# Performance work log

Hardware: AMD Instinct MI355X
Metric: run time of the kernel (lower is better)

## Reference

```python
import jax, jax.numpy as jnp
import numpy as np

B, L, D = 2, 2048, 2048
H, KVH, HD, FD = 8, 1, 256, 64   # heads, kv heads, head_dim, feature_dim
CHUNK = 64


def setup_inputs() -> dict:
    key = jax.random.key(0)
    ks = jax.random.split(key, 8)
    hidden_states = jax.random.normal(ks[0], (B, L, D), dtype=jnp.float32)
    # Gemma-style RoPE tables over half the head dim
    half = HD // 2
    inv_freq = 1.0 / (10000.0 ** (jnp.arange(half, dtype=jnp.float32) / half))
    ang = jnp.arange(L, dtype=jnp.float32)[:, None] * inv_freq[None, :]  # [L, half]
    freqs_cos, freqs_sin = jnp.cos(ang), jnp.sin(ang)
    mask = jnp.ones((1, 1, L, L), dtype=bool)  # unused in linear path
    s = 0.02
    Wq = jax.random.normal(ks[1], (D, H * HD), dtype=jnp.float32) * s
    Wk = jax.random.normal(ks[2], (D, KVH * HD), dtype=jnp.float32) * s
    Wv = jax.random.normal(ks[3], (D, KVH * HD), dtype=jnp.float32) * s
    Wo = jax.random.normal(ks[4], (H * HD, D), dtype=jnp.float32) * s
    fmq = jax.random.normal(ks[5], (H, HD, FD), dtype=jnp.float32) * s
    fmk = jax.random.normal(ks[6], (H, HD, FD), dtype=jnp.float32) * s
    return dict(hidden_states=hidden_states, freqs_cos=freqs_cos, freqs_sin=freqs_sin,
                mask=mask, Wq=Wq, Wk=Wk, Wv=Wv, Wo=Wo, fmq=fmq, fmk=fmk)


def _rope(x, cos, sin):
    # x: [B, L, h, HD]; Gemma complex RoPE: first half = real, second half = imag
    half = x.shape[-1] // 2
    x1, x2 = x[..., :half], x[..., half:]
    c = cos[None, :, None, :]
    s = sin[None, :, None, :]
    return jnp.concatenate([x1 * c - x2 * s, x1 * s + x2 * c], axis=-1)


def _hedgehog(x, W):
    # x: [B, H, L, HD], W: [H, HD, FD] -> softmax over cat([xW, -xW]) -> [B,H,L,2*FD]
    p = jnp.einsum('bhld,hdf->bhlf', x, W)
    return jax.nn.softmax(jnp.concatenate([p, -p], axis=-1), axis=-1)


def _chunk_linear_attn(q, k, v, chunk=CHUNK):
    # q,k: [B,H,L,F]; v: [B,H,L,HD]; chunked causal linear attention
    b, h, l, f = q.shape
    dv = v.shape[-1]
    n = l // chunk
    q = q.reshape(b, h, n, chunk, f) * (f ** -0.5)
    k = k.reshape(b, h, n, chunk, f)
    v = v.reshape(b, h, n, chunk, dv)
    kv = jnp.einsum('bhncf,bhncd->bhnfd', k, v)            # per-chunk KV
    kv = jnp.cumsum(kv, axis=2)
    kv = jnp.concatenate([jnp.zeros_like(kv[:, :, :1]), kv[:, :, :-1]], axis=2)  # exclusive prefix
    inter = jnp.einsum('bhncf,bhnfd->bhncd', q, kv)        # cross-chunk term
    s = jnp.einsum('bhnif,bhnjf->bhnij', q, k)             # intra-chunk scores
    tri = jnp.tril(jnp.ones((chunk, chunk), dtype=bool))
    s = jnp.where(tri, s, 0.0)
    intra = jnp.einsum('bhnij,bhnjd->bhnid', s, v)
    return (inter + intra).reshape(b, h, l, dv)


def reference(hidden_states, freqs_cos, freqs_sin, mask, Wq, Wk, Wv, Wo, fmq, fmk):
    b, l, _ = hidden_states.shape
    q = (hidden_states @ Wq).reshape(b, l, H, HD)
    k = (hidden_states @ Wk).reshape(b, l, KVH, HD)
    v = (hidden_states @ Wv).reshape(b, l, KVH, HD)
    q = _rope(q, freqs_cos, freqs_sin)
    k = _rope(k, freqs_cos, freqs_sin)
    # repeat_interleave kv heads to num_heads (MQA expansion)
    rep = H // KVH
    k = jnp.repeat(k, rep, axis=2)
    v = jnp.repeat(v, rep, axis=2)
    q = jnp.transpose(q, (0, 2, 1, 3))  # [B,H,L,HD]
    k = jnp.transpose(k, (0, 2, 1, 3))
    v = jnp.transpose(v, (0, 2, 1, 3))
    q = _hedgehog(q, fmq)
    k = _hedgehog(k, fmk)
    o = _chunk_linear_attn(q, k, v)                         # [B,H,L,HD]
    o = jnp.transpose(o, (0, 2, 1, 3)).reshape(b, l, H * HD)
    return o @ Wo
```

## Files before the change

### kernel.cpp

```cpp
#include <hip/hip_runtime.h>

#define B_ 2
#define L_ 2048
#define D_ 2048
#define H_ 8
#define HD_ 256
#define FD_ 64
#define F_ 128
#define NC_ 32
#define M_ (B_*L_)
#define SCALE_Q 0.08838834764831845f

typedef unsigned short u16;
typedef __attribute__((ext_vector_type(8))) short bf16x8;
typedef __attribute__((ext_vector_type(8))) unsigned short u16x8;
typedef __attribute__((ext_vector_type(16))) float f32x16;
typedef __attribute__((ext_vector_type(4))) unsigned int u32x4;

#define FMA4(a_, s_, v_) { (a_).x += (s_)*(v_).x; (a_).y += (s_)*(v_).y; \
                           (a_).z += (s_)*(v_).z; (a_).w += (s_)*(v_).w; }


__device__ __forceinline__ u16 bf16_rne(float x) {
  unsigned u = __float_as_uint(x);
  return (u16)((u + 0x7fffu + ((u >> 16) & 1u)) >> 16);
}
__device__ __forceinline__ void bf16_split(float x, u16& h, u16& l) {
  unsigned u = __float_as_uint(x);
  unsigned hb = (u + 0x7fffu + ((u >> 16) & 1u)) >> 16;
  h = (u16)hb;
  float hf = __uint_as_float(hb << 16);
  l = bf16_rne(x - hf);
}

__device__ __forceinline__ void gl_lds16(const u16* g, u16* l) {
  __builtin_amdgcn_global_load_lds(
      (const __attribute__((address_space(1))) unsigned int*)g,
      (__attribute__((address_space(3))) unsigned int*)l, 16, 0, 0);
}

__device__ __forceinline__ size_t kvb_off(int d, int f) {
  return (size_t)(((d >> 7) & 1) * 16384 + ((f >> 5) & 3) * 4096 +
                  ((d >> 6) & 1) * 2048 + ((f >> 4) & 1) * 1024 +
                  ((d >> 5) & 1) * 512 + ((f >> 3) & 1) * 256 +
                  (d & 31) * 8 + (f & 7));
}
__device__ __forceinline__ size_t vb_off(int d, int j) {
  return (size_t)(((d >> 7) & 1) * 8192 + ((j >> 5) & 1) * 4096 +
                  ((d >> 6) & 1) * 2048 + ((j >> 4) & 1) * 1024 +
                  ((d >> 5) & 1) * 512 + ((j >> 3) & 1) * 256 +
                  (d & 31) * 8 + (j & 7));
}

__device__ __forceinline__ void wtrans_body(const float* __restrict__ W, int Nsrc,
                                            int n0, u16* __restrict__ dst,
                                            int P, int kt) {
  int t = threadIdx.x;
  int nn = t & 127, kh = t >> 7;
  const float* src = W + (size_t)(kt * 32 + kh * 16) * Nsrc + n0 + nn;
  u16x8 u0, u1;
  #pragma unroll
  for (int kk = 0; kk < 8; ++kk) u0[kk] = bf16_rne(src[(size_t)kk * Nsrc]);
  #pragma unroll
  for (int kk = 0; kk < 8; ++kk) u1[kk] = bf16_rne(src[(size_t)(kk + 8) * Nsrc]);
  size_t base = ((size_t)P * 64 + kt) * 4096 + (size_t)((nn >> 6) & 1) * 2048
              + (size_t)kh * 1024 + (size_t)((nn >> 5) & 1) * 512
              + (size_t)(nn & 31) * 8;
  *(u16x8*)(dst + base) = u0;
  *(u16x8*)(dst + base + 256) = u1;
}

__global__ __launch_bounds__(256)
void prep_kernel(const float* __restrict__ hs,
                 const float* __restrict__ Wq, const float* __restrict__ Wk,
                 const float* __restrict__ Wv, const float* __restrict__ Wo,
                 u16* __restrict__ hsHt, u16* __restrict__ hsLt,
                 u16* __restrict__ WTh, u16* __restrict__ WoTh) {
  int bid = blockIdx.x;
  if (bid < 4096) {
    int gid = bid * 256 + threadIdx.x;
    int r = gid >> 8, u = gid & 255;
    const float* src = hs + (size_t)r * 2048 + u * 8;
    float4 v0 = *(const float4*)src, v1 = *(const float4*)(src + 4);
    float vals[8] = {v0.x, v0.y, v0.z, v0.w, v1.x, v1.y, v1.z, v1.w};
    u16x8 hv, lv;
    #pragma unroll
    for (int j = 0; j < 8; ++j) { u16 hh, ll; bf16_split(vals[j], hh, ll); hv[j] = hh; lv[j] = ll; }
    size_t off = ((size_t)(r >> 6) * 64 + (u >> 2)) * 2048
               + (size_t)((u >> 1) & 1) * 1024 + (size_t)((r >> 5) & 1) * 512
               + (size_t)(u & 1) * 256 + (size_t)(r & 31) * 8;
    *(u16x8*)(hsHt + off) = hv;
    *(u16x8*)(hsLt + off) = lv;
  } else if (bid < 5376) {
    int idx = bid - 4096;
    int P = idx >> 6, kt = idx & 63;
    const float* W; int Nsrc, n0;
    if (P < 16)      { W = Wq; Nsrc = 2048; n0 = P * 128; }
    else if (P < 18) { W = Wk; Nsrc = 256;  n0 = (P - 16) * 128; }
    else             { W = Wv; Nsrc = 256;  n0 = (P - 18) * 128; }
    wtrans_body(W, Nsrc, n0, WTh, P, kt);
  } else {
    int idx = bid - 5376;
    wtrans_body(Wo, 2048, (idx >> 6) * 128, WoTh, idx >> 6, idx & 63);
  }
}

__global__ __launch_bounds__(256)
void wtrans_wo(const float* __restrict__ Wo, u16* __restrict__ WoTh) {
  wtrans_body(Wo, 2048, blockIdx.x * 128, WoTh, blockIdx.x, blockIdx.y);
}

__device__ __forceinline__ void mfma_body(
    const u16* __restrict__ AtH, const u16* __restrict__ AtL,
    const u16* __restrict__ Bt, float* __restrict__ C, int cstride,
    int bm, int bn) {
  __shared__ __align__(16) u16 AsH[2048];
  __shared__ __align__(16) u16 AsL[2048];
  __shared__ __align__(16) u16 Bs[4096];
  const int t = threadIdx.x, lane = t & 63, wv = t >> 6;
  const u16* aSrc = (wv ? AtL : AtH) + (size_t)bm * 131072 + lane * 8;
  const u16* bSrc = Bt + (size_t)bn * 262144 + wv * 2048 + lane * 8;
  u16* aDst = wv ? AsL : AsH;
  u16* bDst = Bs + wv * 2048;

  f32x16 acc[2][2];
  #pragma unroll
  for (int a = 0; a < 2; ++a)
    #pragma unroll
    for (int b2 = 0; b2 < 2; ++b2)
      #pragma unroll
      for (int r = 0; r < 16; ++r) acc[a][b2][r] = 0.f;

  for (int kt = 0; kt < 64; ++kt) {
    const u16* ak = aSrc + (size_t)kt * 2048;
    const u16* bk = bSrc + (size_t)kt * 4096;
    __syncthreads();
    #pragma unroll
    for (int c = 0; c < 4; ++c) {
      gl_lds16(ak + c * 512, aDst + c * 512);
      gl_lds16(bk + c * 512, bDst + c * 512);
    }
    __syncthreads();

    #pragma unroll
    for (int ks = 0; ks < 2; ++ks) {
      const u16* ph = AsH + ks * 1024 + lane * 8;
      const u16* pl = AsL + ks * 1024 + lane * 8;
      const u16* pb = Bs + wv * 2048 + ks * 1024 + lane * 8;
      bf16x8 a0 = *(const bf16x8*)ph;
      bf16x8 a1 = *(const bf16x8*)(ph + 512);
      bf16x8 b0 = *(const bf16x8*)pb;
      bf16x8 b1 = *(const bf16x8*)(pb + 512);
      acc[0][0] = __builtin_amdgcn_mfma_f32_32x32x16_bf16(a0, b0, acc[0][0], 0, 0, 0);
      acc[0][1] = __builtin_amdgcn_mfma_f32_32x32x16_bf16(a0, b1, acc[0][1], 0, 0, 0);
      acc[1][0] = __builtin_amdgcn_mfma_f32_32x32x16_bf16(a1, b0, acc[1][0], 0, 0, 0);
      acc[1][1] = __builtin_amdgcn_mfma_f32_32x32x16_bf16(a1, b1, acc[1][1], 0, 0, 0);
      bf16x8 l0 = *(const bf16x8*)pl;
      bf16x8 l1 = *(const bf16x8*)(pl + 512);
      acc[0][0] = __builtin_amdgcn_mfma_f32_32x32x16_bf16(l0, b0, acc[0][0], 0, 0, 0);
      acc[0][1] = __builtin_amdgcn_mfma_f32_32x32x16_bf16(l0, b1, acc[0][1], 0, 0, 0);
      acc[1][0] = __builtin_amdgcn_mfma_f32_32x32x16_bf16(l1, b0, acc[1][0], 0, 0, 0);
      acc[1][1] = __builtin_amdgcn_mfma_f32_32x32x16_bf16(l1, b1, acc[1][1], 0, 0, 0);
    }
  }

  const int fr = lane & 31, g = lane >> 5;
  float* Cp = C + (size_t)(bm * 64) * cstride + wv * 64;
  #pragma unroll
  for (int mt = 0; mt < 2; ++mt)
    #pragma unroll
    for (int nt = 0; nt < 2; ++nt) {
      #pragma unroll
      for (int r = 0; r < 16; ++r) {
        int row = mt * 32 + (r & 3) + 8 * (r >> 2) + 4 * g;
        Cp[(size_t)row * cstride + nt * 32 + fr] = acc[mt][nt][r];
      }
    }
}

#define SUB_ 12288
#define MFB(a_, b_, c_) (c_) = __builtin_amdgcn_mfma_f32_32x32x16_bf16((a_), (b_), (c_), 0, 0, 0)

__device__ __forceinline__ void mfma_big_body(
    const u16* __restrict__ AtH, const u16* __restrict__ AtL,
    const u16* __restrict__ Bt, float* __restrict__ C, int cstride,
    int bm, int bn) {
  __shared__ __align__(16) u16 lds[3 * SUB_];
  const int t = threadIdx.x, lane = t & 63, wv = t >> 6;
  const int wm = wv >> 1, wn = wv & 1;

  const u16* gs[6];
  unsigned lo[6], gst[6];
  #pragma unroll
  for (int j = 0; j < 6; ++j) {
    int line = wv * 6 + j;
    if (line < 8) {
      gs[j] = AtH + ((size_t)(2 * bm + (line >> 2)) * 64) * 2048
                  + (size_t)(line & 3) * 512 + lane * 8;
      gst[j] = 2048;
    } else if (line < 16) {
      int l2 = line - 8;
      gs[j] = AtL + ((size_t)(2 * bm + (l2 >> 2)) * 64) * 2048
                  + (size_t)(l2 & 3) * 512 + lane * 8;
      gst[j] = 2048;
    } else {
      int l3 = line - 16;
      gs[j] = Bt + (size_t)bn * 262144 + (size_t)l3 * 512 + lane * 8;
      gst[j] = 4096;
    }
    lo[j] = line * 512;
  }

  f32x16 acc[2][2];
  #pragma unroll
  for (int a = 0; a < 2; ++a)
    #pragma unroll
    for (int b2 = 0; b2 < 2; ++b2)
      #pragma unroll
      for (int r = 0; r < 16; ++r) acc[a][b2][r] = 0.f;

  #pragma unroll
  for (int j = 0; j < 6; ++j) gl_lds16(gs[j], lds + lo[j]);
  #pragma unroll
  for (int j = 0; j < 6; ++j) gl_lds16(gs[j] + gst[j], lds + SUB_ + lo[j]);
  asm volatile("s_waitcnt vmcnt(6)" ::: "memory");
  __builtin_amdgcn_s_barrier();
  __builtin_amdgcn_sched_barrier(0);

  int cb = 0;
  for (int kt = 0; kt < 64; ++kt) {
    int sb = cb + 2 * SUB_; if (sb >= 3 * SUB_) sb -= 3 * SUB_;
    const u16* base = lds + cb;
    const u16* ph0 = base + wm * 2048 + lane * 8;
    const u16* pb0 = base + 8192 + wn * 2048 + lane * 8;

    bf16x8 a0 = *(const bf16x8*)(ph0);
    bf16x8 a1 = *(const bf16x8*)(ph0 + 512);
    bf16x8 l0 = *(const bf16x8*)(ph0 + 4096);
    bf16x8 l1 = *(const bf16x8*)(ph0 + 4608);
    bf16x8 b0 = *(const bf16x8*)(pb0);
    bf16x8 b1 = *(const bf16x8*)(pb0 + 512);
    if (kt < 62) {
      gl_lds16(gs[0] + (size_t)(kt + 2) * gst[0], lds + sb + lo[0]);
      gl_lds16(gs[1] + (size_t)(kt + 2) * gst[1], lds + sb + lo[1]);
      gl_lds16(gs[2] + (size_t)(kt + 2) * gst[2], lds + sb + lo[2]);
    }
    __builtin_amdgcn_s_barrier();
    asm volatile("s_waitcnt lgkmcnt(0)" ::: "memory");
    __builtin_amdgcn_sched_barrier(0);
    __builtin_amdgcn_s_setprio(1);
    MFB(a0, b0, acc[0][0]); MFB(a0, b1, acc[0][1]);
    MFB(a1, b0, acc[1][0]); MFB(a1, b1, acc[1][1]);
    MFB(l0, b0, acc[0][0]); MFB(l0, b1, acc[0][1]);
    MFB(l1, b0, acc[1][0]); MFB(l1, b1, acc[1][1]);
    __builtin_amdgcn_s_setprio(0);
    __builtin_amdgcn_s_barrier();
    __builtin_amdgcn_sched_barrier(0);

    bf16x8 c0 = *(const bf16x8*)(ph0 + 1024);
    bf16x8 c1 = *(const bf16x8*)(ph0 + 1536);
    bf16x8 m0 = *(const bf16x8*)(ph0 + 5120);
    bf16x8 m1 = *(const bf16x8*)(ph0 + 5632);
    bf16x8 d0 = *(const bf16x8*)(pb0 + 1024);
    bf16x8 d1 = *(const bf16x8*)(pb0 + 1536);
    if (kt < 62) {
      gl_lds16(gs[3] + (size_t)(kt + 2) * gst[3], lds + sb + lo[3]);
      gl_lds16(gs[4] + (size_t)(kt + 2) * gst[4], lds + sb + lo[4]);
      gl_lds16(gs[5] + (size_t)(kt + 2) * gst[5], lds + sb + lo[5]);
    }
    __builtin_amdgcn_s_barrier();
    asm volatile("s_waitcnt lgkmcnt(0)" ::: "memory");
    __builtin_amdgcn_sched_barrier(0);
    __builtin_amdgcn_s_setprio(1);
    MFB(c0, d0, acc[0][0]); MFB(c0, d1, acc[0][1]);
    MFB(c1, d0, acc[1][0]); MFB(c1, d1, acc[1][1]);
    MFB(m0, d0, acc[0][0]); MFB(m0, d1, acc[0][1]);
    MFB(m1, d0, acc[1][0]); MFB(m1, d1, acc[1][1]);
    __builtin_amdgcn_s_setprio(0);
    if (kt < 62) asm volatile("s_waitcnt vmcnt(6)" ::: "memory");
    else         asm volatile("s_waitcnt vmcnt(0)" ::: "memory");
    __builtin_amdgcn_s_barrier();
    __builtin_amdgcn_sched_barrier(0);
    cb += SUB_; if (cb == 3 * SUB_) cb = 0;
  }

  const int fr = lane & 31, g = lane >> 5;
  float* Cp = C + (size_t)(bm * 128 + wm * 64) * cstride + wn * 64;
  #pragma unroll
  for (int mt = 0; mt < 2; ++mt)
    #pragma unroll
    for (int nt = 0; nt < 2; ++nt) {
      #pragma unroll
      for (int r = 0; r < 16; ++r) {
        int row = mt * 32 + (r & 3) + 8 * (r >> 2) + 4 * g;
        Cp[(size_t)row * cstride + nt * 32 + fr] = acc[mt][nt][r];
      }
    }
}

__global__ __launch_bounds__(256, 2)
void mfma_q(const u16* __restrict__ hsHt, const u16* __restrict__ hsLt,
            const u16* __restrict__ WTh, float* __restrict__ q) {
  mfma_big_body(hsHt, hsLt, WTh, q + blockIdx.x * 128, 2048,
                blockIdx.y, blockIdx.x);
}

__global__ __launch_bounds__(128, 4)
void mfma_kv(const u16* __restrict__ hsHt, const u16* __restrict__ hsLt,
             const u16* __restrict__ WTh,
             float* __restrict__ k, float* __restrict__ v) {
  int bn = blockIdx.x;
  float* Cb; int co;
  if (bn < 2) { Cb = k; co = bn * 128; }
  else        { Cb = v; co = (bn - 2) * 128; }
  mfma_body(hsHt, hsLt, WTh, Cb + co, 256, blockIdx.y, 16 + bn);
}

__global__ __launch_bounds__(256, 2)
void mfma_wo(const u16* __restrict__ oHt, const u16* __restrict__ oLt,
             const u16* __restrict__ WoTh, float* __restrict__ out) {
  mfma_big_body(oHt, oLt, WoTh, out + blockIdx.x * 128, 2048,
                blockIdx.y, blockIdx.x);
}

__device__ __forceinline__ float wave_max64(float v) {
  #pragma unroll
  for (int off = 32; off > 0; off >>= 1) v = fmaxf(v, __shfl_xor(v, off, 64));
  return v;
}
__device__ __forceinline__ float wave_sum64(float v) {
  #pragma unroll
  for (int off = 32; off > 0; off >>= 1) v += __shfl_xor(v, off, 64);
  return v;
}

__global__ __launch_bounds__(256)
void hedgehog_kernel(const float* __restrict__ q, const float* __restrict__ kx,
                     const float* __restrict__ fmq, const float* __restrict__ fmk,
                     const float* __restrict__ cosb, const float* __restrict__ sinb,
                     float* __restrict__ qf, float* __restrict__ kf,
                     const float* __restrict__ vsrc,
                     u16* __restrict__ vbH, u16* __restrict__ vbL) {
  int bid = blockIdx.x;
  if (bid >= 4096) {
    int bn = bid - 4096;
    const float* vp = vsrc + (size_t)bn * 64 * HD_;
    size_t cbout = (size_t)bn * 16384;
    int d = threadIdx.x;
    #pragma unroll
    for (int it = 0; it < 8; ++it) {
      int j0 = it * 8;
      u16x8 hv, lv;
      #pragma unroll
      for (int c = 0; c < 8; ++c) {
        u16 hh, ll; bf16_split(vp[(size_t)(j0 + c) * HD_ + d], hh, ll);
        hv[c] = hh; lv[c] = ll;
      }
      size_t off = cbout + vb_off(d, j0);
      *(u16x8*)(vbH + off) = hv;
      *(u16x8*)(vbL + off) = lv;
    }
    return;
  }
  __shared__ __align__(16) float rows[4][4][256];
  const float* x; const float* fm; float* out; int nh_in, gb;
  if (bid < 2048) { x = q;  fm = fmq; out = qf; nh_in = 8; gb = bid * 4; }
  else            { x = kx; fm = fmk; out = kf; nh_in = 1; gb = (bid - 2048) * 4; }
  int wave = threadIdx.x >> 6, lane = threadIdx.x & 63;
  int g = gb + wave;
  int l4 = g & (L_/4 - 1);
  int bh = g / (L_/4);
  int h = bh & 7, b = bh >> 3;
  int l0 = l4 * 4;
  size_t rstride = (nh_in == 1) ? (size_t)HD_ : (size_t)H_ * HD_;
  const float* xrow = (nh_in == 1)
      ? x + (size_t)(b * L_ + l0) * HD_
      : x + ((size_t)(b * L_ + l0) * H_ + h) * HD_;
  int dd = (lane & 31) * 4;
  #pragma unroll
  for (int r = 0; r < 4; ++r) {
    float4 v = *(const float4*)(xrow + r * rstride + lane * 4);
    float4 u;
    u.x = __shfl_xor(v.x, 32, 64); u.y = __shfl_xor(v.y, 32, 64);
    u.z = __shfl_xor(v.z, 32, 64); u.w = __shfl_xor(v.w, 32, 64);
    int l = l0 + r;
    float4 c = *(const float4*)(cosb + (size_t)l * 128 + dd);
    float4 s = *(const float4*)(sinb + (size_t)l * 128 + dd);
    float4 ro;
    if (lane < 32) {
      ro.x = v.x * c.x - u.x * s.x; ro.y = v.y * c.y - u.y * s.y;
      ro.z = v.z * c.z - u.z * s.z; ro.w = v.w * c.w - u.w * s.w;
    } else {
      ro.x = u.x * s.x + v.x * c.x; ro.y = u.y * s.y + v.y * c.y;
      ro.z = u.z * s.z + v.z * c.z; ro.w = u.w * s.w + v.w * c.w;
    }
    *(float4*)&rows[wave][r][lane * 4] = ro;
  }
  __syncthreads();

  const float* fmh = fm + (size_t)h * HD_ * FD_;
  float p0 = 0.f, p1 = 0.f, p2 = 0.f, p3 = 0.f;
  for (int d2 = 0; d2 < HD_; d2 += 4) {
    float w0 = fmh[(d2 + 0) * FD_ + lane];
    float w1 = fmh[(d2 + 1) * FD_ + lane];
    float w2 = fmh[(d2 + 2) * FD_ + lane];
    float w3 = fmh[(d2 + 3) * FD_ + lane];
    float4 r0 = *(const float4*)&rows[wave][0][d2];
    float4 r1 = *(const float4*)&rows[wave][1][d2];
    float4 r2 = *(const float4*)&rows[wave][2][d2];
    float4 r3 = *(const float4*)&rows[wave][3][d2];
    p0 += r0.x * w0 + r0.y * w1 + r0.z * w2 + r0.w * w3;
    p1 += r1.x * w0 + r1.y * w1 + r1.z * w2 + r1.w * w3;
    p2 += r2.x * w0 + r2.y * w1 + r2.z * w2 + r2.w * w3;
    p3 += r3.x * w0 + r3.y * w1 + r3.z * w2 + r3.w * w3;
  }
  float p[4] = {p0, p1, p2, p3};
  #pragma unroll
  for (int r = 0; r < 4; ++r) {
    float m = wave_max64(fabsf(p[r]));
    float e1 = __expf(p[r] - m);
    float e2 = __expf(-p[r] - m);
    float z = wave_sum64(e1 + e2);
    float inv = 1.0f / z;
    size_t base = ((size_t)bh * L_ + l0 + r) * F_;
    out[base + lane]      = e1 * inv;
    out[base + 64 + lane] = e2 * inv;
  }
}

__global__ __launch_bounds__(256)
void chunk_kv_kernel(const float* __restrict__ kf, const float* __restrict__ v,
                     u16* __restrict__ kvbH, u16* __restrict__ kvbL) {
  __shared__ __align__(16) float kfs[64][128];
  int n = blockIdx.x & (NC_ - 1), bh = blockIdx.x >> 5;
  int b = bh >> 3;
  const float* kfp = kf + ((size_t)bh * L_ + (size_t)n * 64) * F_;
  int t = threadIdx.x;
  #pragma unroll
  for (int it = 0; it < 8; ++it) {
    int flat = t * 4 + it * 1024;
    *(float4*)&kfs[flat >> 7][flat & 127] = *(const float4*)(kfp + flat);
  }
  __syncthreads();
  int dg = t & 63;
  int fg = t >> 6;
  const float* vp = v + (size_t)(b * L_ + n * 64) * HD_ + dg * 4;
  size_t cb = (size_t)blockIdx.x * 32768;
  #pragma unroll
  for (int pass = 0; pass < 4; ++pass) {
    int f0 = fg * 8 + pass * 32;
    float4 acc[8];
    #pragma unroll
    for (int i = 0; i < 8; ++i) acc[i] = make_float4(0.f, 0.f, 0.f, 0.f);
    for (int j = 0; j < 64; ++j) {
      float4 vv = *(const float4*)(vp + (size_t)j * HD_);
      float4 ka = *(const float4*)&kfs[j][f0];
      float4 kb = *(const float4*)&kfs[j][f0 + 4];
      FMA4(acc[0], ka.x, vv); FMA4(acc[1], ka.y, vv);
      FMA4(acc[2], ka.z, vv); FMA4(acc[3], ka.w, vv);
      FMA4(acc[4], kb.x, vv); FMA4(acc[5], kb.y, vv);
      FMA4(acc[6], kb.z, vv); FMA4(acc[7], kb.w, vv);
    }
    #pragma unroll
    for (int c = 0; c < 4; ++c) {
      u16x8 hv, lv;
      #pragma unroll
      for (int ff = 0; ff < 8; ++ff) {
        float xs = (c == 0) ? acc[ff].x : (c == 1) ? acc[ff].y
                 : (c == 2) ? acc[ff].z : acc[ff].w;
        u16 hh, ll; bf16_split(xs, hh, ll); hv[ff] = hh; lv[ff] = ll;
      }
      int d = dg * 4 + c;
      size_t off = cb + kvb_off(d, f0);
      *(u16x8*)(kvbH + off) = hv;
      *(u16x8*)(kvbL + off) = lv;
    }
  }
}

__global__ __launch_bounds__(256)
void chunk_scan_kernel(u16* __restrict__ kvbH, u16* __restrict__ kvbL) {
  int bh = blockIdx.x >> 4, g = blockIdx.x & 15;
  int d = threadIdx.x;
  size_t off = kvb_off(d, g * 8);
  float run[8] = {0.f, 0.f, 0.f, 0.f, 0.f, 0.f, 0.f, 0.f};
  for (int n = 0; n < NC_; ++n) {
    size_t a = ((size_t)(bh * 32 + n)) * 32768 + off;
    u16x8 hv = *(u16x8*)(kvbH + a);
    u16x8 lv = *(u16x8*)(kvbL + a);
    u16x8 oh, ol;
    #pragma unroll
    for (int c = 0; c < 8; ++c) {
      float val = __uint_as_float((unsigned)hv[c] << 16)
                + __uint_as_float((unsigned)lv[c] << 16);
      u16 hh, ll; bf16_split(run[c], hh, ll); oh[c] = hh; ol[c] = ll;
      run[c] += val;
    }
    *(u16x8*)(kvbH + a) = oh;
    *(u16x8*)(kvbL + a) = ol;
  }
}

__global__ __launch_bounds__(256, 2)
void chunk_attn_kernel(const float* __restrict__ qf, const float* __restrict__ kf,
                       const u16* __restrict__ vbH, const u16* __restrict__ vbL,
                       const u16* __restrict__ kvbH, const u16* __restrict__ kvbL,
                       u16* __restrict__ oHt, u16* __restrict__ oLt) {
  __shared__ __align__(16) u16 lds[32768];
  const int n = blockIdx.x & (NC_ - 1), bh = blockIdx.x >> 5;
  const int h = bh & 7, b = bh >> 3;
  const int t = threadIdx.x;
  const int w = t >> 6, i31 = t & 31, G = (t >> 5) & 1;
  const int l8 = (t & 63) * 8;

  {
    const float* qp = qf + ((size_t)bh * L_ + (size_t)n * 64) * F_;
    const float* kp = kf + ((size_t)bh * L_ + (size_t)n * 64) * F_;
    int o8 = t & 15, ib = t >> 4;
    #pragma unroll
    for (int iter = 0; iter < 4; ++iter) {
      int i = ib + iter * 16;
      int it = i >> 5, ks = o8 >> 1;
      int sub = (it * 8 + ks) * 512 + (o8 & 1) * 256 + (i & 31) * 8;
      {
        const float* src = qp + (size_t)i * 128 + o8 * 8;
        float4 a = *(const float4*)src, c = *(const float4*)(src + 4);
        float vals[8] = {a.x, a.y, a.z, a.w, c.x, c.y, c.z, c.w};
        u16x8 hv, lv;
        #pragma unroll
        for (int j = 0; j < 8; ++j) {
          u16 hh, ll; bf16_split(vals[j] * SCALE_Q, hh, ll);
          hv[j] = hh; lv[j] = ll;
        }
        *(u16x8*)(lds + sub) = hv;
        *(u16x8*)(lds + 8192 + sub) = lv;
      }
      {
        const float* src = kp + (size_t)i * 128 + o8 * 8;
        float4 a = *(const float4*)src, c = *(const float4*)(src + 4);
        float vals[8] = {a.x, a.y, a.z, a.w, c.x, c.y, c.z, c.w};
        u16x8 hv, lv;
        #pragma unroll
        for (int j = 0; j < 8; ++j) {
          u16 hh, ll; bf16_split(vals[j], hh, ll);
          hv[j] = hh; lv[j] = ll;
        }
        *(u16x8*)(lds + 16384 + sub) = hv;
        *(u16x8*)(lds + 24576 + sub) = lv;
      }
    }
  }
  __syncthreads();

  const u16* Lq  = lds;
  const u16* Lql = lds + 8192;
  const u16* Lk  = lds + 16384;
  const u16* Lkl = lds + 24576;

  f32x16 st[2][2];
  #pragma unroll
  for (int a = 0; a < 2; ++a)
    #pragma unroll
    for (int c = 0; c < 2; ++c)
      #pragma unroll
      for (int r = 0; r < 16; ++r) st[a][c][r] = 0.f;

  #pragma unroll
  for (int ks = 0; ks < 8; ++ks) {
    bf16x8 kh0 = *(const bf16x8*)(Lk  + ks * 512 + l8);
    bf16x8 kh1 = *(const bf16x8*)(Lk  + (8 + ks) * 512 + l8);
    bf16x8 kl0 = *(const bf16x8*)(Lkl + ks * 512 + l8);
    bf16x8 kl1 = *(const bf16x8*)(Lkl + (8 + ks) * 512 + l8);
    bf16x8 qh0 = *(const bf16x8*)(Lq  + ks * 512 + l8);
    bf16x8 qh1 = *(const bf16x8*)(Lq  + (8 + ks) * 512 + l8);
    bf16x8 ql0 = *(const bf16x8*)(Lql + ks * 512 + l8);
    bf16x8 ql1 = *(const bf16x8*)(Lql + (8 + ks) * 512 + l8);
    MFB(kh0, qh0, st[0][0]); MFB(kh0, ql0, st[0][0]); MFB(kl0, qh0, st[0][0]);
    MFB(kh0, qh1, st[0][1]); MFB(kh0, ql1, st[0][1]); MFB(kl0, qh1, st[0][1]);
    MFB(kh1, qh0, st[1][0]); MFB(kh1, ql0, st[1][0]); MFB(kl1, qh0, st[1][0]);
    MFB(kh1, qh1, st[1][1]); MFB(kh1, ql1, st[1][1]); MFB(kl1, qh1, st[1][1]);
  }

  bf16x8 sfH[2][4], sfL[2][4];
  #pragma unroll
  for (int mt = 0; mt < 2; ++mt) {
    int iv = mt * 32 + i31;
    #pragma unroll
    for (int ksj = 0; ksj < 4; ++ksj) {
      const int jt = ksj >> 1, kb = ksj & 1;
      unsigned ph[4], pl[4];
      #pragma unroll
      for (int half = 0; half < 2; ++half) {
        u16 hh[4], ll[4];
        #pragma unroll
        for (int c = 0; c < 4; ++c) {
          int r = 8 * kb + 4 * half + c;
          int jv = jt * 32 + (r & 3) + 8 * (r >> 2) + 4 * G;
          float mv = (jv <= iv) ? st[jt][mt][r] : 0.f;
          u16 h_, l_; bf16_split(mv, h_, l_);
          hh[c] = h_; ll[c] = l_;
        }
        ph[half * 2 + 0] = (unsigned)hh[0] | ((unsigned)hh[1] << 16);
        ph[half * 2 + 1] = (unsigned)hh[2] | ((unsigned)hh[3] << 16);
        pl[half * 2 + 0] = (unsigned)ll[0] | ((unsigned)ll[1] << 16);
        pl[half * 2 + 1] = (unsigned)ll[2] | ((unsigned)ll[3] << 16);
      }
      unsigned rH1 = (unsigned)__shfl_xor((int)(G ? ph[0] : ph[2]), 32, 64);
      unsigned rH2 = (unsigned)__shfl_xor((int)(G ? ph[1] : ph[3]), 32, 64);
      unsigned rL1 = (unsigned)__shfl_xor((int)(G ? pl[0] : pl[2]), 32, 64);
      unsigned rL2 = (unsigned)__shfl_xor((int)(G ? pl[1] : pl[3]), 32, 64);
      u32x4 wH, wL;
      wH[0] = G ? rH1 : ph[0]; wH[1] = G ? rH2 : ph[1];
      wH[2] = G ? ph[2] : rH1; wH[3] = G ? ph[3] : rH2;
      wL[0] = G ? rL1 : pl[0]; wL[1] = G ? rL2 : pl[1];
      wL[2] = G ? pl[2] : rL1; wL[3] = G ? pl[3] : rL2;
      sfH[mt][ksj] = __builtin_bit_cast(bf16x8, wH);
      sfL[mt][ksj] = __builtin_bit_cast(bf16x8, wL);
    }
  }

  f32x16 acc[2][2];
  #pragma unroll
  for (int a = 0; a < 2; ++a)
    #pragma unroll
    for (int c = 0; c < 2; ++c)
      #pragma unroll
      for (int r = 0; r < 16; ++r) acc[a][c][r] = 0.f;

  {
    size_t vcb = ((size_t)(b * NC_ + n)) * 16384;
    #pragma unroll
    for (int nt = 0; nt < 2; ++nt) {
      #pragma unroll
      for (int ksj = 0; ksj < 4; ++ksj) {
        size_t basev = vcb + vb_off(w * 64 + nt * 32, ksj * 16) + l8;
        bf16x8 vH = *(const bf16x8*)((const short*)(vbH + basev));
        bf16x8 vL = *(const bf16x8*)((const short*)(vbL + basev));
        MFB(sfH[0][ksj], vH, acc[0][nt]); MFB(sfL[0][ksj], vH, acc[0][nt]);
        MFB(sfH[0][ksj], vL, acc[0][nt]);
        MFB(sfH[1][ksj], vH, acc[1][nt]); MFB(sfL[1][ksj], vH, acc[1][nt]);
        MFB(sfH[1][ksj], vL, acc[1][nt]);
      }
    }
  }

  {
    size_t cb = (size_t)blockIdx.x * 32768;
    #pragma unroll
    for (int ks = 0; ks < 8; ++ks) {
      bf16x8 qa_h0 = *(const bf16x8*)(Lq  + ks * 512 + l8);
      bf16x8 qa_h1 = *(const bf16x8*)(Lq  + (8 + ks) * 512 + l8);
      bf16x8 qa_l0 = *(const bf16x8*)(Lql + ks * 512 + l8);
      bf16x8 qa_l1 = *(const bf16x8*)(Lql + (8 + ks) * 512 + l8);
      #pragma unroll
      for (int nt = 0; nt < 2; ++nt) {
        size_t base = cb + kvb_off(w * 64 + nt * 32, ks * 16) + l8;
        bf16x8 kvH = *(const bf16x8*)((const short*)(kvbH + base));
        bf16x8 kvL = *(const bf16x8*)((const short*)(kvbL + base));
        MFB(qa_h0, kvH, acc[0][nt]); MFB(qa_l0, kvH, acc[0][nt]);
        MFB(qa_h0, kvL, acc[0][nt]);
        MFB(qa_h1, kvH, acc[1][nt]); MFB(qa_l1, kvH, acc[1][nt]);
        MFB(qa_h1, kvL, acc[1][nt]);
      }
    }
  }

  {
    int p = b * NC_ + n;
    #pragma unroll
    for (int mt = 0; mt < 2; ++mt)
      #pragma unroll
      for (int nt = 0; nt < 2; ++nt) {
        int u_ = h * 32 + w * 8 + nt * 4 + (i31 >> 3);
        size_t ob = ((size_t)p * 64 + (u_ >> 2)) * 2048
                  + (size_t)((u_ >> 1) & 1) * 1024 + (size_t)mt * 512
                  + (size_t)(u_ & 1) * 256 + (size_t)(i31 & 7);
        #pragma unroll
        for (int r = 0; r < 16; ++r) {
          int rr = (r & 3) + 8 * (r >> 2) + 4 * G;
          u16 hh, ll; bf16_split(acc[mt][nt][r], hh, ll);
          oHt[ob + (size_t)rr * 8] = hh;
          oLt[ob + (size_t)rr * 8] = ll;
        }
      }
  }
}

extern "C" void kernel_launch(void* const* d_in, const int* in_sizes, int n_in,
                              void* d_out, int out_size, void* d_ws, size_t ws_size,
                              hipStream_t stream) {
  const float* hs   = (const float*)d_in[0];
  const float* fcos = (const float*)d_in[1];
  const float* fsin = (const float*)d_in[2];
  const float* Wq  = (const float*)d_in[4];
  const float* Wk  = (const float*)d_in[5];
  const float* Wv  = (const float*)d_in[6];
  const float* Wo  = (const float*)d_in[7];
  const float* fmq = (const float*)d_in[8];
  const float* fmk = (const float*)d_in[9];
  float* out = (float*)d_out;

  float* ws = (float*)d_ws;
  float* q  = ws;
  float* k  = q  + (size_t)M_ * 2048;
  float* v  = k  + (size_t)M_ * 256;
  float* qf = v  + (size_t)M_ * 256;
  float* kf = qf + (size_t)B_ * H_ * L_ * F_;
  float* kvr = kf + (size_t)B_ * H_ * L_ * F_;

  u16* hsHt = (u16*)kvr;
  u16* hsLt = hsHt + (size_t)M_ * 2048;
  u16* WTh  = hsLt + (size_t)M_ * 2048;
  u16* kvbH = (u16*)kvr;
  u16* kvbL = kvbH + (size_t)512 * 32768;
  u16* vbH  = (u16*)k;
  u16* vbL  = vbH + (size_t)64 * 16384;
  u16* oHt  = (u16*)q;
  u16* oLt  = oHt + (size_t)M_ * 2048;

  const size_t WS_BASE = (size_t)142606336;
  bool bigws = ws_size >= WS_BASE + (size_t)8388608;
  u16* WoTh = bigws ? (u16*)((char*)d_ws + WS_BASE) : (u16*)kvr;

  prep_kernel<<<bigws ? 6400 : 5376, 256, 0, stream>>>(
      hs, Wq, Wk, Wv, Wo, hsHt, hsLt, WTh, WoTh);
  mfma_q<<<dim3(16, 32), 256, 0, stream>>>(hsHt, hsLt, WTh, q);
  mfma_kv<<<dim3(4, 64), 128, 0, stream>>>(hsHt, hsLt, WTh, k, v);
  hedgehog_kernel<<<4096 + 64, 256, 0, stream>>>(q, k, fmq, fmk, fcos, fsin,
                                                 qf, kf, v, vbH, vbL);
  chunk_kv_kernel<<<B_ * H_ * NC_, 256, 0, stream>>>(kf, v, kvbH, kvbL);
  chunk_scan_kernel<<<256, 256, 0, stream>>>(kvbH, kvbL);
  chunk_attn_kernel<<<B_ * H_ * NC_, 256, 0, stream>>>(qf, kf, vbH, vbL,
                                                       kvbH, kvbL, oHt, oLt);
  if (!bigws)
    wtrans_wo<<<dim3(16, 64), 256, 0, stream>>>(Wo, WoTh);
  mfma_wo<<<dim3(16, 32), 256, 0, stream>>>(oHt, oLt, WoTh, out);
}
```

Baseline: 490.2 us.

## Compute hedgehog feature-map projection with split-bf16 MFMA instead of scalar FMAs

Replaces the scalar hedgehog kernel, where each wave handled four rows with per-lane FMA loops, with an MFMA kernel. Each block does RoPE on 128 rows, splits them into hi/lo bf16 in LDS, and multiplies by pre-split feature-map weights using three bf16 MFMAs to keep near-fp32 accuracy. The softmax then runs across 32-lane groups on the accumulator layout. The feature-map weights are pre-transposed and split in prep_kernel. The v bf16 conversion moves to a separate workspace region so it does not alias k, with a fallback kernel when the workspace is small. The block count drops from 4096 to 512 with a large 128KB LDS footprint, which limits occupancy.

```diff
diff --git a/kernel.cpp b/kernel.cpp
--- a/kernel.cpp
+++ b/kernel.cpp
@@ -14,6 +14,7 @@
 typedef unsigned short u16;
 typedef __attribute__((ext_vector_type(8))) short bf16x8;
 typedef __attribute__((ext_vector_type(8))) unsigned short u16x8;
+typedef __attribute__((ext_vector_type(4))) unsigned short u16x4;
 typedef __attribute__((ext_vector_type(16))) float f32x16;
 typedef __attribute__((ext_vector_type(4))) unsigned int u32x4;
 
@@ -74,8 +75,10 @@
 void prep_kernel(const float* __restrict__ hs,
                  const float* __restrict__ Wq, const float* __restrict__ Wk,
                  const float* __restrict__ Wv, const float* __restrict__ Wo,
+                 const float* __restrict__ fmq, const float* __restrict__ fmk,
                  u16* __restrict__ hsHt, u16* __restrict__ hsLt,
-                 u16* __restrict__ WTh, u16* __restrict__ WoTh) {
+                 u16* __restrict__ WTh, u16* __restrict__ WoTh,
+                 u16* __restrict__ fmbtH, u16* __restrict__ fmbtL) {
   int bid = blockIdx.x;
   if (bid < 4096) {
     int gid = bid * 256 + threadIdx.x;
@@ -99,8 +102,26 @@
     else if (P < 18) { W = Wk; Nsrc = 256;  n0 = (P - 16) * 128; }
     else             { W = Wv; Nsrc = 256;  n0 = (P - 18) * 128; }
     wtrans_body(W, Nsrc, n0, WTh, P, kt);
+  } else if (bid < 5504) {
+    int idx = bid - 5376;
+    int h16 = idx >> 3, kt = idx & 7;
+    const float* src = (h16 < 8) ? (fmq + (size_t)h16 * 16384)
+                                 : (fmk + (size_t)(h16 - 8) * 16384);
+    int t = threadIdx.x;
+    int f = t & 63, kq = t >> 6;
+    u16x8 hv, lv;
+    #pragma unroll
+    for (int i = 0; i < 8; ++i) {
+      float val = src[(size_t)(kt * 32 + kq * 8 + i) * 64 + f];
+      u16 hh, ll; bf16_split(val, hh, ll); hv[i] = hh; lv[i] = ll;
+    }
+    size_t base = (size_t)(h16 * 8 + kt) * 2048 + (size_t)(kq >> 1) * 1024
+                + (size_t)(f >> 5) * 512 + (size_t)(kq & 1) * 256
+                + (size_t)(f & 31) * 8;
+    *(u16x8*)(fmbtH + base) = hv;
+    *(u16x8*)(fmbtL + base) = lv;
   } else {
-    int idx = bid - 5376;
+    int idx = bid - 5504;
     wtrans_body(Wo, 2048, (idx >> 6) * 128, WoTh, idx >> 6, idx & 63);
   }
 }
@@ -108,6 +129,28 @@
 __global__ __launch_bounds__(256)
 void wtrans_wo(const float* __restrict__ Wo, u16* __restrict__ WoTh) {
   wtrans_body(Wo, 2048, blockIdx.x * 128, WoTh, blockIdx.x, blockIdx.y);
+}
+
+__global__ __launch_bounds__(256)
+void prep_v(const float* __restrict__ v, u16* __restrict__ vbH,
+            u16* __restrict__ vbL) {
+  int bn = blockIdx.x;
+  const float* vp = v + (size_t)bn * 64 * HD_;
+  size_t cbout = (size_t)bn * 16384;
+  int d = threadIdx.x;
+  #pragma unroll
+  for (int it = 0; it < 8; ++it) {
+    int j0 = it * 8;
+    u16x8 hv, lv;
+    #pragma unroll
+    for (int c = 0; c < 8; ++c) {
+      u16 hh, ll; bf16_split(vp[(size_t)(j0 + c) * HD_ + d], hh, ll);
+      hv[c] = hh; lv[c] = ll;
+    }
+    size_t off = cbout + vb_off(d, j0);
+    *(u16x8*)(vbH + off) = hv;
+    *(u16x8*)(vbL + off) = lv;
+  }
 }
 
 __device__ __forceinline__ void mfma_body(
@@ -323,27 +366,16 @@
                 blockIdx.y, blockIdx.x);
 }
 
-__device__ __forceinline__ float wave_max64(float v) {
-  #pragma unroll
-  for (int off = 32; off > 0; off >>= 1) v = fmaxf(v, __shfl_xor(v, off, 64));
-  return v;
-}
-__device__ __forceinline__ float wave_sum64(float v) {
-  #pragma unroll
-  for (int off = 32; off > 0; off >>= 1) v += __shfl_xor(v, off, 64);
-  return v;
-}
-
-__global__ __launch_bounds__(256)
-void hedgehog_kernel(const float* __restrict__ q, const float* __restrict__ kx,
-                     const float* __restrict__ fmq, const float* __restrict__ fmk,
-                     const float* __restrict__ cosb, const float* __restrict__ sinb,
-                     float* __restrict__ qf, float* __restrict__ kf,
-                     const float* __restrict__ vsrc,
-                     u16* __restrict__ vbH, u16* __restrict__ vbL) {
+__global__ __launch_bounds__(256, 1)
+void mfma_hh(const float* __restrict__ q, const float* __restrict__ kx,
+             const float* __restrict__ cosb, const float* __restrict__ sinb,
+             const u16* __restrict__ fmbtH, const u16* __restrict__ fmbtL,
+             float* __restrict__ qf, float* __restrict__ kf,
+             const float* __restrict__ vsrc,
+             u16* __restrict__ vbH, u16* __restrict__ vbL) {
   int bid = blockIdx.x;
-  if (bid >= 4096) {
-    int bn = bid - 4096;
+  if (bid >= 512) {
+    int bn = bid - 512;
     const float* vp = vsrc + (size_t)bn * 64 * HD_;
     size_t cbout = (size_t)bn * 16384;
     int d = threadIdx.x;
@@ -362,69 +394,97 @@
     }
     return;
   }
-  __shared__ __align__(16) float rows[4][4][256];
-  const float* x; const float* fm; float* out; int nh_in, gb;
-  if (bid < 2048) { x = q;  fm = fmq; out = qf; nh_in = 8; gb = bid * 4; }
-  else            { x = kx; fm = fmk; out = kf; nh_in = 1; gb = (bid - 2048) * 4; }
-  int wave = threadIdx.x >> 6, lane = threadIdx.x & 63;
-  int g = gb + wave;
-  int l4 = g & (L_/4 - 1);
-  int bh = g / (L_/4);
-  int h = bh & 7, b = bh >> 3;
-  int l0 = l4 * 4;
-  size_t rstride = (nh_in == 1) ? (size_t)HD_ : (size_t)H_ * HD_;
-  const float* xrow = (nh_in == 1)
-      ? x + (size_t)(b * L_ + l0) * HD_
-      : x + ((size_t)(b * L_ + l0) * H_ + h) * HD_;
-  int dd = (lane & 31) * 4;
-  #pragma unroll
-  for (int r = 0; r < 4; ++r) {
-    float4 v = *(const float4*)(xrow + r * rstride + lane * 4);
-    float4 u;
-    u.x = __shfl_xor(v.x, 32, 64); u.y = __shfl_xor(v.y, 32, 64);
-    u.z = __shfl_xor(v.z, 32, 64); u.w = __shfl_xor(v.w, 32, 64);
-    int l = l0 + r;
-    float4 c = *(const float4*)(cosb + (size_t)l * 128 + dd);
-    float4 s = *(const float4*)(sinb + (size_t)l * 128 + dd);
-    float4 ro;
-    if (lane < 32) {
-      ro.x = v.x * c.x - u.x * s.x; ro.y = v.y * c.y - u.y * s.y;
-      ro.z = v.z * c.z - u.z * s.z; ro.w = v.w * c.w - u.w * s.w;
-    } else {
-      ro.x = u.x * s.x + v.x * c.x; ro.y = u.y * s.y + v.y * c.y;
-      ro.z = u.z * s.z + v.z * c.z; ro.w = u.w * s.w + v.w * c.w;
-    }
-    *(float4*)&rows[wave][r][lane * 4] = ro;
+  __shared__ __align__(16) u16 xlds[65536];
+  const int t = threadIdx.x;
+  const int rt = bid & 31, h16 = bid >> 5;
+  const int rowbase = rt * 128;
+  const float* xsrc; size_t xstr;
+  if (h16 < 8) { xsrc = q + (size_t)h16 * 256; xstr = 2048; }
+  else         { xsrc = kx;                    xstr = 256; }
+
+  for (int iter = 0; iter < 16; ++iter) {
+    int flat = iter * 1024 + t * 4;
+    int r = flat >> 7, dd = flat & 127;
+    int grow = rowbase + r;
+    int l = grow & 2047;
+    const float* xr = xsrc + (size_t)grow * xstr + dd;
+    float4 x1 = *(const float4*)xr;
+    float4 x2 = *(const float4*)(xr + 128);
+    float4 c  = *(const float4*)(cosb + (size_t)l * 128 + dd);
+    float4 s  = *(const float4*)(sinb + (size_t)l * 128 + dd);
+    float lo4[4] = {x1.x*c.x - x2.x*s.x, x1.y*c.y - x2.y*s.y,
+                    x1.z*c.z - x2.z*s.z, x1.w*c.w - x2.w*s.w};
+    float hi4[4] = {x1.x*s.x + x2.x*c.x, x1.y*s.y + x2.y*c.y,
+                    x1.z*s.z + x2.z*c.z, x1.w*s.w + x2.w*c.w};
+    int rt32 = r >> 5, r5 = r & 31;
+    #pragma unroll
+    for (int half = 0; half < 2; ++half) {
+      int d = dd + half * 128;
+      int kt = d >> 5, k = d & 31;
+      unsigned base = (unsigned)((kt * 4 + rt32) * 2) * 1024
+                    + (unsigned)(k >> 4) * 512 + (unsigned)((k >> 3) & 1) * 256
+                    + (unsigned)r5 * 8 + (unsigned)(k & 7);
+      const float* vv = half ? hi4 : lo4;
+      u16x4 hv, lv;
+      #pragma unroll
+      for (int j = 0; j < 4; ++j) {
+        u16 hh, ll; bf16_split(vv[j], hh, ll); hv[j] = hh; lv[j] = ll;
+      }
+      *(u16x4*)(xlds + base) = hv;
+      *(u16x4*)(xlds + 1024 + base) = lv;
+    }
   }
   __syncthreads();
 
-  const float* fmh = fm + (size_t)h * HD_ * FD_;
-  float p0 = 0.f, p1 = 0.f, p2 = 0.f, p3 = 0.f;
-  for (int d2 = 0; d2 < HD_; d2 += 4) {
-    float w0 = fmh[(d2 + 0) * FD_ + lane];
-    float w1 = fmh[(d2 + 1) * FD_ + lane];
-    float w2 = fmh[(d2 + 2) * FD_ + lane];
-    float w3 = fmh[(d2 + 3) * FD_ + lane];
-    float4 r0 = *(const float4*)&rows[wave][0][d2];
-    float4 r1 = *(const float4*)&rows[wave][1][d2];
-    float4 r2 = *(const float4*)&rows[wave][2][d2];
-    float4 r3 = *(const float4*)&rows[wave][3][d2];
-    p0 += r0.x * w0 + r0.y * w1 + r0.z * w2 + r0.w * w3;
-    p1 += r1.x * w0 + r1.y * w1 + r1.z * w2 + r1.w * w3;
-    p2 += r2.x * w0 + r2.y * w1 + r2.z * w2 + r2.w * w3;
-    p3 += r3.x * w0 + r3.y * w1 + r3.z * w2 + r3.w * w3;
-  }
-  float p[4] = {p0, p1, p2, p3};
-  #pragma unroll
-  for (int r = 0; r < 4; ++r) {
-    float m = wave_max64(fabsf(p[r]));
-    float e1 = __expf(p[r] - m);
-    float e2 = __expf(-p[r] - m);
-    float z = wave_sum64(e1 + e2);
-    float inv = 1.0f / z;
-    size_t base = ((size_t)bh * L_ + l0 + r) * F_;
-    out[base + lane]      = e1 * inv;
-    out[base + 64 + lane] = e2 * inv;
+  const int w = t >> 6, lane = t & 63;
+  f32x16 acc[2];
+  #pragma unroll
+  for (int nt = 0; nt < 2; ++nt)
+    #pragma unroll
+    for (int r = 0; r < 16; ++r) acc[nt][r] = 0.f;
+
+  const u16* fmbH = fmbtH + (size_t)h16 * 8 * 2048;
+  const u16* fmbL = fmbtL + (size_t)h16 * 8 * 2048;
+  #pragma unroll
+  for (int kt = 0; kt < 8; ++kt) {
+    unsigned xb = (unsigned)((kt * 4 + w) * 2) * 1024;
+    #pragma unroll
+    for (int ks = 0; ks < 2; ++ks) {
+      bf16x8 xh = *(const bf16x8*)(xlds + xb + ks * 512 + lane * 8);
+      bf16x8 xl = *(const bf16x8*)(xlds + xb + 1024 + ks * 512 + lane * 8);
+      #pragma unroll
+      for (int nt = 0; nt < 2; ++nt) {
+        size_t fb = (size_t)kt * 2048 + ks * 1024 + nt * 512 + lane * 8;
+        bf16x8 bh_ = *(const bf16x8*)((const short*)(fmbH + fb));
+        bf16x8 bl_ = *(const bf16x8*)((const short*)(fmbL + fb));
+        MFB(xh, bh_, acc[nt]); MFB(xl, bh_, acc[nt]); MFB(xh, bl_, acc[nt]);
+      }
+    }
+  }
+
+  const int g = lane >> 5, f31 = lane & 31;
+  float* outp = (h16 < 8) ? qf : kf;
+  const int hh = h16 & 7;
+  #pragma unroll
+  for (int r = 0; r < 16; ++r) {
+    int rowl = (r & 3) + 8 * (r >> 2) + 4 * g;
+    int grow = rowbase + w * 32 + rowl;
+    float p0 = acc[0][r], p1 = acc[1][r];
+    float m = fmaxf(fabsf(p0), fabsf(p1));
+    #pragma unroll
+    for (int off = 16; off > 0; off >>= 1) m = fmaxf(m, __shfl_xor(m, off, 64));
+    float e0 = __expf(p0 - m),  e0n = __expf(-p0 - m);
+    float e1 = __expf(p1 - m),  e1n = __expf(-p1 - m);
+    float zl = e0 + e0n + e1 + e1n;
+    #pragma unroll
+    for (int off = 16; off > 0; off >>= 1) zl += __shfl_xor(zl, off, 64);
+    float inv = 1.0f / zl;
+    int b = grow >> 11, l = grow & 2047;
+    size_t ob = ((size_t)((b * 8 + hh) * 2048 + l)) * 128;
+    outp[ob + f31]       = e0 * inv;
+    outp[ob + 32 + f31]  = e1 * inv;
+    outp[ob + 64 + f31]  = e0n * inv;
+    outp[ob + 96 + f31]  = e1n * inv;
   }
 }
 
@@ -711,23 +771,27 @@
   u16* hsHt = (u16*)kvr;
   u16* hsLt = hsHt + (size_t)M_ * 2048;
   u16* WTh  = hsLt + (size_t)M_ * 2048;
+  u16* fmbtH = WTh + (size_t)1280 * 4096;
+  u16* fmbtL = fmbtH + (size_t)131072 * 2;
   u16* kvbH = (u16*)kvr;
   u16* kvbL = kvbH + (size_t)512 * 32768;
-  u16* vbH  = (u16*)k;
-  u16* vbL  = vbH + (size_t)64 * 16384;
   u16* oHt  = (u16*)q;
   u16* oLt  = oHt + (size_t)M_ * 2048;
 
   const size_t WS_BASE = (size_t)142606336;
-  bool bigws = ws_size >= WS_BASE + (size_t)8388608;
+  bool bigws = ws_size >= WS_BASE + (size_t)12582912;
   u16* WoTh = bigws ? (u16*)((char*)d_ws + WS_BASE) : (u16*)kvr;
-
-  prep_kernel<<<bigws ? 6400 : 5376, 256, 0, stream>>>(
-      hs, Wq, Wk, Wv, Wo, hsHt, hsLt, WTh, WoTh);
+  u16* vbH  = bigws ? (u16*)((char*)d_ws + WS_BASE + 8388608) : (u16*)k;
+  u16* vbL  = vbH + (size_t)64 * 16384;
+
+  prep_kernel<<<bigws ? 6528 : 5504, 256, 0, stream>>>(
+      hs, Wq, Wk, Wv, Wo, fmq, fmk, hsHt, hsLt, WTh, WoTh, fmbtH, fmbtL);
   mfma_q<<<dim3(16, 32), 256, 0, stream>>>(hsHt, hsLt, WTh, q);
   mfma_kv<<<dim3(4, 64), 128, 0, stream>>>(hsHt, hsLt, WTh, k, v);
-  hedgehog_kernel<<<4096 + 64, 256, 0, stream>>>(q, k, fmq, fmk, fcos, fsin,
-                                                 qf, kf, v, vbH, vbL);
+  mfma_hh<<<bigws ? 576 : 512, 256, 0, stream>>>(
+      q, k, fcos, fsin, fmbtH, fmbtL, qf, kf, v, vbH, vbL);
+  if (!bigws)
+    prep_v<<<B_ * NC_, 256, 0, stream>>>(v, vbH, vbL);
   chunk_kv_kernel<<<B_ * H_ * NC_, 256, 0, stream>>>(kf, v, kvbH, kvbL);
   chunk_scan_kernel<<<256, 256, 0, stream>>>(kvbH, kvbL);
   chunk_attn_kernel<<<B_ * H_ * NC_, 256, 0, stream>>>(qf, kf, vbH, vbL,
```

Measured after the change: 481.2 us (median of 2 runs). No clear change (-1.8%).
